# Kernel optimization log

Measured on AMD Instinct MI355X. Metric: run time of the kernel, lower is better.

## Reference

```python
import jax, jax.numpy as jnp
import numpy as np

N, DX, DZ, DY, H = 8192, 64, 128, 16, 512


def setup_inputs() -> dict:
    key = jax.random.key(0)
    ks = jax.random.split(key, 8)
    s1 = 1.0 / np.sqrt(DX)
    s2 = 1.0 / np.sqrt(H)
    return {
        "z_pred": jax.random.normal(ks[0], (N, DZ), dtype=jnp.float32),
        "x_label": jax.random.normal(ks[1], (N, DX), dtype=jnp.float32),
        "y_label": jax.random.normal(ks[2], (N, DY), dtype=jnp.float32),
        "W1": jax.random.normal(ks[3], (DX, H), dtype=jnp.float32) * s1,
        "b1": jnp.zeros((H,), dtype=jnp.float32),
        "W2": jax.random.normal(ks[4], (H, DZ), dtype=jnp.float32) * s2,
        "b2": jnp.zeros((DZ,), dtype=jnp.float32),
        "A": jax.random.normal(ks[5], (DZ, DZ), dtype=jnp.float32) * (1.0 / np.sqrt(DZ)),
        "B": jax.random.normal(ks[6], (DZ, DY), dtype=jnp.float32) * (1.0 / np.sqrt(DY)),
    }


def reference(z_pred, x_label, y_label, W1, b1, W2, b2, A, B):
    # forward_mapper T: x (dx,) -> (dz,), 2-layer tanh MLP
    def T(x):
        return jnp.tanh(x @ W1 + b1) @ W2 + b2

    # diff_eq: per-sample nonlinear dynamics x_dot = tanh(x)
    x_dot = jnp.tanh(x_label)  # (N, dx)

    # per-sample Jacobian dT/dx: (N, dz, dx). Equivalent to the torch code's
    # full N x N batched Jacobian followed by the diagonal slice, but without
    # the O(N^2) waste.
    jac = jax.vmap(jax.jacrev(T))(x_label)  # (N, dz, dx)

    dtdx_mul_f = jnp.einsum("nzd,nd->nz", jac, x_dot)  # (N, dz)
    m_mul_t = z_pred @ A.T                              # (N, dz)
    k_mul_h = y_label @ B.T                             # (N, dz)

    pde = dtdx_mul_f - m_mul_t - k_mul_h                # (N, dz)
    loss_batch = jnp.linalg.norm(pde, axis=1)           # (N,)
    return jnp.mean(loss_batch)
```

## Files before the change

kernel.cpp:

```cpp
#include <hip/hip_runtime.h>
#include <math.h>

#define Nn   8192
#define DXc  64
#define DZc  128
#define DYc  16
#define Hc   512
#define NKC  21

typedef short bf16x8 __attribute__((ext_vector_type(8)));
typedef float f32x4  __attribute__((ext_vector_type(4)));

__device__ __forceinline__ float fast_tanh(float x) {
    float e = __expf(2.0f * x);
    return 1.0f - 2.0f / (e + 1.0f);
}
__device__ __forceinline__ short f2bf(float f) {
    unsigned u = __float_as_uint(f);
    return (short)((u + 0x7FFFu + ((u >> 16) & 1u)) >> 16);
}
__device__ __forceinline__ bf16x8 pack8(float4 a, float4 b) {
    bf16x8 r;
    r[0]=f2bf(a.x); r[1]=f2bf(a.y); r[2]=f2bf(a.z); r[3]=f2bf(a.w);
    r[4]=f2bf(b.x); r[5]=f2bf(b.y); r[6]=f2bf(b.z); r[7]=f2bf(b.w);
    return r;
}

__global__ __launch_bounds__(256)
void prep_kernel(const float* __restrict__ W1,
                 const float* __restrict__ W2,
                 const float* __restrict__ A,
                 const float* __restrict__ Bm,
                 short* __restrict__ Wb,
                 short* __restrict__ Wf,
                 float* __restrict__ out) {
    int c = blockIdx.x * 256 + threadIdx.x;
    if (c == 0) out[0] = 0.f;

    if (c < 4096) {
        int lane = c & 63, block = c >> 6;
        int n16 = lane & 15, q = lane >> 4;
        int j = (block >> 1) * 16 + n16;
        int k0 = (block & 1) * 32 + q * 8;
        bf16x8 v;
#pragma unroll
        for (int i = 0; i < 8; i++) v[i] = f2bf(W1[(size_t)(k0 + i) * Hc + j]);
        *(bf16x8*)(Wb + (size_t)c * 8) = v;
    } else {
        int c2 = c - 4096;
        int lane = c2 & 63, block = c2 >> 6;
        int zt = block / 21, kc = block % 21;
        int n16 = lane & 15, q = lane >> 4;
        int z = zt * 16 + n16;
        bf16x8 v = (bf16x8){0,0,0,0,0,0,0,0};
        if (kc < 16) {
            int k0 = kc * 32 + q * 8;
#pragma unroll
            for (int i = 0; i < 8; i++) v[i] = f2bf(W2[(size_t)(k0 + i) * DZc + z]);
        } else if (kc < 20) {
            int c0 = (kc - 16) * 32 + q * 8;
            float4 a0 = *(const float4*)(A + (size_t)z * DZc + c0);
            float4 a1 = *(const float4*)(A + (size_t)z * DZc + c0 + 4);
            v[0]=f2bf(-a0.x); v[1]=f2bf(-a0.y); v[2]=f2bf(-a0.z); v[3]=f2bf(-a0.w);
            v[4]=f2bf(-a1.x); v[5]=f2bf(-a1.y); v[6]=f2bf(-a1.z); v[7]=f2bf(-a1.w);
        } else if (q < 2) {
            float4 b0 = *(const float4*)(Bm + (size_t)z * DYc + q * 8);
            float4 b1 = *(const float4*)(Bm + (size_t)z * DYc + q * 8 + 4);
            v[0]=f2bf(-b0.x); v[1]=f2bf(-b0.y); v[2]=f2bf(-b0.z); v[3]=f2bf(-b0.w);
            v[4]=f2bf(-b1.x); v[5]=f2bf(-b1.y); v[6]=f2bf(-b1.z); v[7]=f2bf(-b1.w);
        }
        *(bf16x8*)(Wf + (size_t)c2 * 8) = v;
    }
}

#define MFMA16(a, b, c) __builtin_amdgcn_mfma_f32_16x16x32_bf16((a), (b), (c), 0, 0, 0)

__global__ __launch_bounds__(512, 2)
void pde_main(const float* __restrict__ z_pred,
              const float* __restrict__ x_label,
              const float* __restrict__ y_label,
              const float* __restrict__ b1,
              const short* __restrict__ Wb,
              const short* __restrict__ Wf,
              float* __restrict__ out) {
    __shared__ __align__(16) short sS[2][16 * 512];
    __shared__ float red[8][2][16];

    const int tid  = threadIdx.x;
    const int w    = tid >> 6;
    const int lane = tid & 63;
    const int n16  = lane & 15;
    const int q    = lane >> 4;
    const int n0   = blockIdx.x * 32;

    bf16x8 ax0[2], ax1[2], at0[2], at1[2];
#pragma unroll
    for (int g = 0; g < 2; g++) {
        const float* xp = x_label + (size_t)(n0 + g * 16 + n16) * DXc + q * 8;
        float4 x0 = *(const float4*)xp,        x1 = *(const float4*)(xp + 4);
        float4 x2 = *(const float4*)(xp + 32), x3 = *(const float4*)(xp + 36);
        ax0[g] = pack8(x0, x1);  ax1[g] = pack8(x2, x3);
        float v[16] = {x0.x,x0.y,x0.z,x0.w, x1.x,x1.y,x1.z,x1.w,
                       x2.x,x2.y,x2.z,x2.w, x3.x,x3.y,x3.z,x3.w};
#pragma unroll
        for (int i = 0; i < 8; i++) { at0[g][i] = f2bf(fast_tanh(v[i])); at1[g][i] = f2bf(fast_tanh(v[8 + i])); }
    }

#pragma unroll
    for (int t = 0; t < 4; t++) {
        const int jt = 4 * w + t;
        const short* bp = Wb + (size_t)(jt * 2 * 64 + lane) * 8;
        bf16x8 bw0 = *(const bf16x8*)bp;
        bf16x8 bw1 = *(const bf16x8*)(bp + 512);
        const float bj = b1[jt * 16 + n16];
        const int j = jt * 16 + n16;
        const int sbase = (j >> 5) * 512 + ((j >> 3) & 3) * 128 + (j & 7);
#pragma unroll
        for (int g = 0; g < 2; g++) {
            f32x4 h = (f32x4){0.f,0.f,0.f,0.f};
            f32x4 u = (f32x4){0.f,0.f,0.f,0.f};
            h = MFMA16(ax0[g], bw0, h);  h = MFMA16(ax1[g], bw1, h);
            u = MFMA16(at0[g], bw0, u);  u = MFMA16(at1[g], bw1, u);
#pragma unroll
            for (int reg = 0; reg < 4; reg++) {
                float tv = fast_tanh(h[reg] + bj);
                float s  = (1.f - tv * tv) * u[reg];
                sS[g][sbase + (q * 4 + reg) * 8] = f2bf(s);
            }
        }
    }

    const short* wfb = Wf + (size_t)(w * NKC * 64 + lane) * 8;
    f32x4 acc[2] = {(f32x4){0.f,0.f,0.f,0.f}, (f32x4){0.f,0.f,0.f,0.f}};
    {
#pragma unroll
        for (int kcl = 0; kcl < 4; kcl++) {
            bf16x8 bz = *(const bf16x8*)(wfb + (16 + kcl) * 512);
#pragma unroll
            for (int g = 0; g < 2; g++) {
                const float* zp = z_pred + (size_t)(n0 + g * 16 + n16) * DZc + kcl * 32 + q * 8;
                bf16x8 az = pack8(*(const float4*)zp, *(const float4*)(zp + 4));
                acc[g] = MFMA16(az, bz, acc[g]);
            }
        }
        bf16x8 by = *(const bf16x8*)(wfb + 20 * 512);
#pragma unroll
        for (int g = 0; g < 2; g++) {
            bf16x8 ay = (bf16x8){0,0,0,0,0,0,0,0};
            if (q < 2) {
                const float* yp = y_label + (size_t)(n0 + g * 16 + n16) * DYc + q * 8;
                ay = pack8(*(const float4*)yp, *(const float4*)(yp + 4));
            }
            acc[g] = MFMA16(ay, by, acc[g]);
        }
    }

    __syncthreads();

#pragma unroll
    for (int kc = 0; kc < 16; kc++) {
        bf16x8 bk = *(const bf16x8*)(wfb + kc * 512);
        bf16x8 sa0 = *(const bf16x8*)(sS[0] + kc * 512 + lane * 8);
        bf16x8 sa1 = *(const bf16x8*)(sS[1] + kc * 512 + lane * 8);
        acc[0] = MFMA16(sa0, bk, acc[0]);
        acc[1] = MFMA16(sa1, bk, acc[1]);
    }

#pragma unroll
    for (int g = 0; g < 2; g++) {
#pragma unroll
        for (int reg = 0; reg < 4; reg++) {
            float sq = acc[g][reg] * acc[g][reg];
            sq += __shfl_xor(sq, 1);
            sq += __shfl_xor(sq, 2);
            sq += __shfl_xor(sq, 4);
            sq += __shfl_xor(sq, 8);
            if (n16 == 0) red[w][g][q * 4 + reg] = sq;
        }
    }
    __syncthreads();

    if (tid < 32) {
        const int g = tid >> 4, r = tid & 15;
        float tot = 0.f;
#pragma unroll
        for (int i = 0; i < 8; i++) tot += red[i][g][r];
        float nrm = sqrtf(tot);
        nrm += __shfl_xor(nrm, 1);
        nrm += __shfl_xor(nrm, 2);
        nrm += __shfl_xor(nrm, 4);
        nrm += __shfl_xor(nrm, 8);
        nrm += __shfl_xor(nrm, 16);
        if (tid == 0) atomicAdd(out, nrm * (1.0f / (float)Nn));
    }
}

extern "C" void kernel_launch(void* const* d_in, const int* in_sizes, int n_in,
                              void* d_out, int out_size, void* d_ws, size_t ws_size,
                              hipStream_t stream) {
    const float* z_pred  = (const float*)d_in[0];
    const float* x_label = (const float*)d_in[1];
    const float* y_label = (const float*)d_in[2];
    const float* W1      = (const float*)d_in[3];
    const float* b1      = (const float*)d_in[4];
    const float* W2      = (const float*)d_in[5];
    const float* A       = (const float*)d_in[7];
    const float* Bm      = (const float*)d_in[8];

    short* Wb = (short*)d_ws;
    short* Wf = Wb + 512 * DXc;

    prep_kernel<<<58, 256, 0, stream>>>(W1, W2, A, Bm, Wb, Wf, (float*)d_out);
    pde_main<<<Nn / 32, 512, 0, stream>>>(z_pred, x_label, y_label, b1, Wb, Wf, (float*)d_out);
}
```

Baseline: 88.34 us.

## Stage x/z/y inputs in LDS once per block and swap MFMA operands

Inputs x_label, z_pred and y_label are now loaded once per block with coalesced, thread-contiguous reads, converted to bf16 (plus tanh for x), and stored in shared memory in MFMA fragment layout. Previously each of the 8 waves reloaded and reconverted the same rows from global memory. The first-layer MFMA swaps the A and B operands so each lane writes 4 contiguous bf16 to the sS buffer with one vector store instead of 4 scalar stores, and b1 is read as a vector. This costs extra LDS space and an additional barrier, which may lower occupancy.

```diff
diff --git a/kernel.cpp b/kernel.cpp
--- a/kernel.cpp
+++ b/kernel.cpp
@@ -9,6 +9,7 @@
 #define NKC  21
 
 typedef short bf16x8 __attribute__((ext_vector_type(8)));
+typedef short bf16x4 __attribute__((ext_vector_type(4)));
 typedef float f32x4  __attribute__((ext_vector_type(4)));
 
 __device__ __forceinline__ float fast_tanh(float x) {
@@ -84,6 +85,10 @@
               const short* __restrict__ Wf,
               float* __restrict__ out) {
     __shared__ __align__(16) short sS[2][16 * 512];
+    __shared__ __align__(16) short xf[2][2 * 512];
+    __shared__ __align__(16) short tf[2][2 * 512];
+    __shared__ __align__(16) short zf[2][4 * 512];
+    __shared__ __align__(16) short yf[2][512];
     __shared__ float red[8][2][16];
 
     const int tid  = threadIdx.x;
@@ -93,40 +98,75 @@
     const int q    = lane >> 4;
     const int n0   = blockIdx.x * 32;
 
-    bf16x8 ax0[2], ax1[2], at0[2], at1[2];
-#pragma unroll
-    for (int g = 0; g < 2; g++) {
-        const float* xp = x_label + (size_t)(n0 + g * 16 + n16) * DXc + q * 8;
-        float4 x0 = *(const float4*)xp,        x1 = *(const float4*)(xp + 4);
-        float4 x2 = *(const float4*)(xp + 32), x3 = *(const float4*)(xp + 36);
-        ax0[g] = pack8(x0, x1);  ax1[g] = pack8(x2, x3);
-        float v[16] = {x0.x,x0.y,x0.z,x0.w, x1.x,x1.y,x1.z,x1.w,
-                       x2.x,x2.y,x2.z,x2.w, x3.x,x3.y,x3.z,x3.w};
-#pragma unroll
-        for (int i = 0; i < 8; i++) { at0[g][i] = f2bf(fast_tanh(v[i])); at1[g][i] = f2bf(fast_tanh(v[8 + i])); }
-    }
+    {
+        const int s  = tid >> 4;
+        const int g  = s >> 4;
+        const int ns = s & 15;
+
+        {
+            const int kc4 = tid & 15;
+            float4 v = *(const float4*)(x_label + (size_t)n0 * DXc + (size_t)tid * 4);
+            const int off = (kc4 >> 3) * 512 + (ns + ((kc4 >> 1) & 3) * 16) * 8 + (kc4 & 1) * 4;
+            bf16x4 xs, ts;
+            xs[0]=f2bf(v.x); xs[1]=f2bf(v.y); xs[2]=f2bf(v.z); xs[3]=f2bf(v.w);
+            ts[0]=f2bf(fast_tanh(v.x)); ts[1]=f2bf(fast_tanh(v.y));
+            ts[2]=f2bf(fast_tanh(v.z)); ts[3]=f2bf(fast_tanh(v.w));
+            *(bf16x4*)&xf[g][off] = xs;
+            *(bf16x4*)&tf[g][off] = ts;
+        }
+
+        {
+            const int kc8 = tid & 15;
+            const float* zp = z_pred + (size_t)n0 * DZc + (size_t)tid * 8;
+            bf16x8 zv = pack8(*(const float4*)zp, *(const float4*)(zp + 4));
+            *(bf16x8*)&zf[g][(kc8 >> 2) * 512 + (ns + (kc8 & 3) * 16) * 8] = zv;
+        }
+
+        if (tid < 64) {
+            const int sy = tid >> 1, ky = tid & 1;
+            const float* yp = y_label + (size_t)(n0 + sy) * DYc + ky * 8;
+            bf16x8 yv = pack8(*(const float4*)yp, *(const float4*)(yp + 4));
+            *(bf16x8*)&yf[sy >> 4][((sy & 15) + ky * 16) * 8] = yv;
+        } else if (tid < 128) {
+            const int t2 = tid - 64;
+            const int sy = t2 >> 1, qy = 2 + (t2 & 1);
+            *(bf16x8*)&yf[sy >> 4][((sy & 15) + qy * 16) * 8] = (bf16x8){0,0,0,0,0,0,0,0};
+        }
+    }
+    __syncthreads();
+
+    bf16x8 bx[2][2], bt[2][2];
+#pragma unroll
+    for (int g = 0; g < 2; g++)
+#pragma unroll
+        for (int kc = 0; kc < 2; kc++) {
+            bx[g][kc] = *(const bf16x8*)&xf[g][kc * 512 + lane * 8];
+            bt[g][kc] = *(const bf16x8*)&tf[g][kc * 512 + lane * 8];
+        }
 
 #pragma unroll
     for (int t = 0; t < 4; t++) {
         const int jt = 4 * w + t;
-        const short* bp = Wb + (size_t)(jt * 2 * 64 + lane) * 8;
-        bf16x8 bw0 = *(const bf16x8*)bp;
-        bf16x8 bw1 = *(const bf16x8*)(bp + 512);
-        const float bj = b1[jt * 16 + n16];
-        const int j = jt * 16 + n16;
-        const int sbase = (j >> 5) * 512 + ((j >> 3) & 3) * 128 + (j & 7);
+        const short* apw = Wb + (size_t)(jt * 2 * 64 + lane) * 8;
+        bf16x8 aw0 = *(const bf16x8*)apw;
+        bf16x8 aw1 = *(const bf16x8*)(apw + 512);
+        f32x4 bj = *(const f32x4*)(b1 + jt * 16 + q * 4);
+        const int soff = (jt >> 1) * 512
+                       + (n16 + ((((jt & 1) << 1) | (q >> 1)) * 16)) * 8
+                       + (q & 1) * 4;
 #pragma unroll
         for (int g = 0; g < 2; g++) {
             f32x4 h = (f32x4){0.f,0.f,0.f,0.f};
             f32x4 u = (f32x4){0.f,0.f,0.f,0.f};
-            h = MFMA16(ax0[g], bw0, h);  h = MFMA16(ax1[g], bw1, h);
-            u = MFMA16(at0[g], bw0, u);  u = MFMA16(at1[g], bw1, u);
-#pragma unroll
-            for (int reg = 0; reg < 4; reg++) {
-                float tv = fast_tanh(h[reg] + bj);
-                float s  = (1.f - tv * tv) * u[reg];
-                sS[g][sbase + (q * 4 + reg) * 8] = f2bf(s);
+            h = MFMA16(aw0, bx[g][0], h);  h = MFMA16(aw1, bx[g][1], h);
+            u = MFMA16(aw0, bt[g][0], u);  u = MFMA16(aw1, bt[g][1], u);
+            bf16x4 sv;
+#pragma unroll
+            for (int r = 0; r < 4; r++) {
+                float tv = fast_tanh(h[r] + bj[r]);
+                sv[r] = f2bf((1.f - tv * tv) * u[r]);
             }
+            *(bf16x4*)&sS[g][soff] = sv;
         }
     }
 
@@ -138,19 +178,14 @@
             bf16x8 bz = *(const bf16x8*)(wfb + (16 + kcl) * 512);
 #pragma unroll
             for (int g = 0; g < 2; g++) {
-                const float* zp = z_pred + (size_t)(n0 + g * 16 + n16) * DZc + kcl * 32 + q * 8;
-                bf16x8 az = pack8(*(const float4*)zp, *(const float4*)(zp + 4));
+                bf16x8 az = *(const bf16x8*)&zf[g][kcl * 512 + lane * 8];
                 acc[g] = MFMA16(az, bz, acc[g]);
             }
         }
         bf16x8 by = *(const bf16x8*)(wfb + 20 * 512);
 #pragma unroll
         for (int g = 0; g < 2; g++) {
-            bf16x8 ay = (bf16x8){0,0,0,0,0,0,0,0};
-            if (q < 2) {
-                const float* yp = y_label + (size_t)(n0 + g * 16 + n16) * DYc + q * 8;
-                ay = pack8(*(const float4*)yp, *(const float4*)(yp + 4));
-            }
+            bf16x8 ay = *(const bf16x8*)&yf[g][lane * 8];
             acc[g] = MFMA16(ay, by, acc[g]);
         }
     }
@@ -160,8 +195,8 @@
 #pragma unroll
     for (int kc = 0; kc < 16; kc++) {
         bf16x8 bk = *(const bf16x8*)(wfb + kc * 512);
-        bf16x8 sa0 = *(const bf16x8*)(sS[0] + kc * 512 + lane * 8);
-        bf16x8 sa1 = *(const bf16x8*)(sS[1] + kc * 512 + lane * 8);
+        bf16x8 sa0 = *(const bf16x8*)&sS[0][kc * 512 + lane * 8];
+        bf16x8 sa1 = *(const bf16x8*)&sS[1][kc * 512 + lane * 8];
         acc[0] = MFMA16(sa0, bk, acc[0]);
         acc[1] = MFMA16(sa1, bk, acc[1]);
     }
```

After: 82.36 us. 6.8% less time.
